# Optimization experiments

Hardware: AMD Instinct MI355X
Metric: run time of the kernel (lower is better)

## Reference

```python
import jax, jax.numpy as jnp
import numpy as np

WINDOW = 20  # window_size from init

def setup_inputs() -> dict:
    key = jax.random.key(0)
    ks = jax.random.split(key, 8)
    B, K, L, H = 8, 64, 1024, 256
    FFN = 3 * H * 4  # input_dim*ffn_ratio
    cand_span_reps = jax.random.normal(ks[0], (B, K, H), dtype=jnp.float32)
    token_reps = jax.random.normal(ks[1], (B, L, H), dtype=jnp.float32)
    W1 = jax.random.normal(ks[2], (3 * H, FFN), dtype=jnp.float32) * (1.0 / np.sqrt(3 * H))
    b1 = jnp.zeros((FFN,), dtype=jnp.float32)
    W2 = jax.random.normal(ks[3], (FFN, H), dtype=jnp.float32) * (1.0 / np.sqrt(FFN))
    b2 = jnp.zeros((H,), dtype=jnp.float32)
    cand_span_ids = jnp.sort(jax.random.randint(ks[4], (B, K, 2), 0, L), axis=-1)
    token_masks = jnp.ones((B, L), dtype=bool)
    return {"cand_span_reps": cand_span_reps, "token_reps": token_reps,
            "W1": W1, "b1": b1, "W2": W2, "b2": b2,
            "cand_span_ids": cand_span_ids, "token_masks": token_masks}

def _span_window_max(token_reps, span_ids, token_masks, window):
    # token_reps: [B,L,H]; span_ids: [B,K,2]; token_masks: [B,L]
    L = token_reps.shape[1]
    seq = jnp.arange(L)[None, None, :]                      # [1,1,L]
    start = span_ids[:, :, 0][:, :, None]                   # [B,K,1]
    end = span_ids[:, :, 1][:, :, None]                     # [B,K,1]
    mask = (((seq >= start - window) & (seq < start)) |
            ((seq > end) & (seq <= end + window)))
    mask = mask & token_masks[:, None, :]                   # [B,K,L]
    # masked max over L -> [B,K,H]
    filled = jnp.where(mask[..., None], token_reps[:, None, :, :], -jnp.inf)
    return jnp.max(filled, axis=2)

def reference(cand_span_reps, token_reps, W1, b1, W2, b2, cand_span_ids, token_masks):
    B, K, H = cand_span_reps.shape
    # Per-span pooled window context [B,K,H]. The pairwise context over the
    # UNION of head & tail windows equals the elementwise max of the two
    # per-span window maxes (max over A|B == max(max A, max B)).
    ctx = _span_window_max(token_reps, cand_span_ids, token_masks, WINDOW)
    context_reps = jnp.maximum(ctx[:, :, None, :], ctx[:, None, :, :])   # [B,K,K,H]
    head_reps = jnp.broadcast_to(cand_span_reps[:, :, None, :], (B, K, K, H))
    tail_reps = jnp.broadcast_to(cand_span_reps[:, None, :, :], (B, K, K, H))
    rel = jnp.concatenate([head_reps, tail_reps, context_reps], axis=-1)  # [B,K,K,3H]
    h = jax.nn.relu(jnp.einsum('bijd,df->bijf', rel, W1) + b1)
    out = jnp.einsum('bijf,fh->bijh', h, W2) + b2
    return out.reshape(B, K * K, H)
```

## Files before the change

kernel.cpp:

```cpp
#include <hip/hip_runtime.h>
#include <hip/hip_bf16.h>
#include <cstdint>
#include <cstddef>


typedef __attribute__((ext_vector_type(8))) short short8;
typedef __attribute__((ext_vector_type(4))) float f32x4;
typedef __attribute__((ext_vector_type(2))) unsigned int u32x2;

#define B_DIM 8
#define K_DIM 64
#define H_DIM 256
#define L_DIM 1024
#define FFN_DIM 3072
#define WINDOW 20

__device__ __forceinline__ unsigned short f2b(float f) {
  unsigned int u = __float_as_uint(f);
  unsigned int r = (u + 0x7FFFu + ((u >> 16) & 1u)) >> 16;
  return (unsigned short)r;
}
__device__ __forceinline__ float b2f(unsigned short h) {
  return __uint_as_float(((unsigned int)h) << 16);
}
__device__ __forceinline__ f32x4 zero4() {
  f32x4 z = {0.f, 0.f, 0.f, 0.f};
  return z;
}
__device__ __forceinline__ void gload_lds16(const void* g, void* l) {
  __builtin_amdgcn_global_load_lds(
      (const __attribute__((address_space(1))) void*)g,
      (__attribute__((address_space(3))) void*)l, 16, 0, 0);
}
__device__ __forceinline__ unsigned int cvt_pk_bf16(float lo, float hi) {
  unsigned int r;
  asm("v_cvt_pk_bf16_f32 %0, %1, %2" : "=v"(r) : "v"(lo), "v"(hi));
  return r;
}


__global__ void cvt_bf16_kernel(const float* __restrict__ in,
                                unsigned short* __restrict__ out, int n) {
  int i = blockIdx.x * blockDim.x + threadIdx.x;
  if (i < n) out[i] = f2b(in[i]);
}

__global__ void transpose_cvt_kernel(const float* __restrict__ in,
                                     unsigned short* __restrict__ out,
                                     int R, int C) {
  __shared__ float t[64][65];
  int c0 = blockIdx.x * 64, r0 = blockIdx.y * 64;
  int tr = threadIdx.x >> 6, tc = threadIdx.x & 63;
  for (int rr = tr; rr < 64; rr += 4)
    t[rr][tc] = in[(size_t)(r0 + rr) * C + (c0 + tc)];
  __syncthreads();
  for (int cc = tr; cc < 64; cc += 4)
    out[(size_t)(c0 + cc) * R + (r0 + tc)] = f2b(t[tc][cc]);
}

__global__ void ctx_kernel(const float* __restrict__ token,
                           const int* __restrict__ ids,
                           unsigned short* __restrict__ ctx) {
  int bk = blockIdx.x;
  int b = bk >> 6;
  int h = threadIdx.x;
  int s = ids[bk * 2 + 0];
  int e = ids[bk * 2 + 1];
  const float* tb = token + ((size_t)b * L_DIM) * H_DIM + h;
  float m = -INFINITY;
  int lo = s - WINDOW; if (lo < 0) lo = 0;
  for (int l2 = lo; l2 < s; ++l2) m = fmaxf(m, tb[(size_t)l2 * H_DIM]);
  int hi = e + WINDOW; if (hi > L_DIM - 1) hi = L_DIM - 1;
  for (int l2 = e + 1; l2 <= hi; ++l2) m = fmaxf(m, tb[(size_t)l2 * H_DIM]);
  ctx[(size_t)bk * H_DIM + h] = f2b(m);
}

__global__ __launch_bounds__(256) void at_gemm_kernel(
    const unsigned short* __restrict__ candb,
    const unsigned short* __restrict__ w1abt,
    const float* __restrict__ b1, float* __restrict__ AT) {
  int n0 = blockIdx.x * 64;
  int r0 = blockIdx.y * 64;
  __shared__ __align__(16) unsigned short A[64 * 256];
  int w = threadIdx.x >> 6, l = threadIdx.x & 63;
  int l15 = l & 15, l4 = l >> 4;
  {
    int row = w * 16 + l15;
    const short8* src = (const short8*)(candb + (size_t)(r0 + row) * H_DIM);
    #pragma unroll
    for (int t = 0; t < 8; ++t) {
      int u = l4 + 4 * t;
      short8 v = src[u];
      *(short8*)(A + row * 256 + ((u ^ (row & 7)) * 8)) = v;
    }
  }
  __syncthreads();
  f32x4 acc[4] = {zero4(), zero4(), zero4(), zero4()};
  int n = n0 + 16 * w + l15;
  const unsigned short* bp = w1abt + (size_t)n * H_DIM + l4 * 8;
  #pragma unroll
  for (int kk = 0; kk < 8; ++kk) {
    short8 bfrag = *(const short8*)(bp + kk * 32);
    #pragma unroll
    for (int rf = 0; rf < 4; ++rf) {
      int row = rf * 16 + l15;
      int u = kk * 4 + l4;
      short8 afrag = *(const short8*)(A + row * 256 + ((u ^ (row & 7)) * 8));
      acc[rf] = __builtin_amdgcn_mfma_f32_16x16x32_bf16(afrag, bfrag, acc[rf], 0, 0, 0);
    }
  }
  float bias = (n < FFN_DIM) ? b1[n] : 0.0f;
  #pragma unroll
  for (int rf = 0; rf < 4; ++rf) {
    #pragma unroll
    for (int qq = 0; qq < 4; ++qq) {
      int row = r0 + rf * 16 + l4 * 4 + qq;
      AT[(size_t)row * (2 * FFN_DIM) + n] = acc[rf][qq] + bias;
    }
  }
}

__global__ __launch_bounds__(1024, 4) void fused_kernel(
    const unsigned short* __restrict__ ctx,
    const unsigned short* __restrict__ w1ct,
    const unsigned short* __restrict__ w2t,
    const float* __restrict__ AT,
    const float* __restrict__ b2,
    float* __restrict__ out) {
  int blk = blockIdx.x;
  blk = (blk & 7) * 32 + (blk >> 3);
  int b = blk >> 5, qp = blk & 31;

  __shared__ __align__(16) char W1s[3 * 16384];
  __shared__ __align__(16) char W2s4[4 * 16384];
  __shared__ __align__(16) char HcS[2 * 8192];

  int tid = threadIdx.x;
  int w = tid >> 6, l = tid & 63;
  int l15 = l & 15, l4 = l >> 4;
  int wl = l15 & 7;
  int s3 = (l15 >> 1) & 3;

  if (w < 8) {
    int wf = w & 1, wj2 = w >> 1;
    int i_w = 2 * qp + (wj2 >> 1);
    int jloc = 32 * (wj2 & 1) + l15;

    short8 bfr[8][2];
    {
      const unsigned short* cb = ctx + ((size_t)b * K_DIM) * H_DIM;
      const unsigned short* ci = cb + (size_t)i_w * H_DIM;
      #pragma unroll
      for (int kk = 0; kk < 8; ++kk) {
        int hoff = kk * 32 + l4 * 8;
        short8 vi = *(const short8*)(ci + hoff);
        #pragma unroll
        for (int jb = 0; jb < 2; ++jb) {
          short8 vj = *(const short8*)(cb + (size_t)(jloc + jb * 16) * H_DIM + hoff);
          short8 vm;
          #pragma unroll
          for (int e = 0; e < 8; ++e) {
            float fa = b2f((unsigned short)vi[e]);
            float fb = b2f((unsigned short)vj[e]);
            vm[e] = (fa >= fb) ? vi[e] : vj[e];
          }
          bfr[kk][jb] = vm;
        }
      }
    }

    int tid_p = (w << 6) | l;
    int fr = tid_p >> 5, u32i = tid_p & 31;
    int offW1 = fr * 512 + (((u32i & 24) | ((u32i & 7) ^ (fr & 7))) << 4);

    int baseA = (16 * wf + l15) * 512;
    int offAe = ((l4 ^ wl) << 4);
    int offAo = (((4 + l4) ^ wl) << 4);
    int colw = 32 * wj2 + l15;
    int uW = 2 * wf + (l4 >> 1);
    int offHw = colw * 64 + ((uW ^ s3) << 4) + ((l4 & 1) << 3);

    const float* avp = AT + (size_t)(b * K_DIM + i_w) * (2 * FFN_DIM) + 16 * wf + 4 * l4;
    const float* tvp = AT + (size_t)(b * K_DIM + jloc) * (2 * FFN_DIM) + FFN_DIM + 16 * wf + 4 * l4;

    auto stageW1 = [&](int c, int buf) {
      const char* g = (const char*)w1ct + (size_t)c * 16384 + offW1;
      char* d = &W1s[buf * 16384 + tid_p * 16];
      gload_lds16(g, d);
      gload_lds16(g + 8192, d + 8192);
    };

    stageW1(0, 0);
    stageW1(1, 1);
    __builtin_amdgcn_sched_barrier(0);
    asm volatile("s_waitcnt vmcnt(2)" ::: "memory");
    __builtin_amdgcn_sched_barrier(0);
    __builtin_amdgcn_s_barrier();
    __builtin_amdgcn_sched_barrier(0);

    int rb = 0, sb = 2;
    for (int c = 0; c <= 96; ++c) {
      f32x4 av = zero4(), tv0 = zero4(), tv1 = zero4();
      if (c < 96) {
        av  = *(const f32x4*)(avp + c * 32);
        tv0 = *(const f32x4*)(tvp + c * 32);
        tv1 = *(const f32x4*)(tvp + 98304 + c * 32);
      }
      __builtin_amdgcn_sched_barrier(0);
      stageW1(c + 2 > 95 ? 95 : c + 2, sb);
      __builtin_amdgcn_sched_barrier(0);

      if (c < 96) {
        const char* w1p = &W1s[rb * 16384 + baseA];
        f32x4 acc1[2] = {zero4(), zero4()};
        __builtin_amdgcn_s_setprio(1);
        #pragma unroll
        for (int m = 0; m < 4; ++m) {
          short8 afe = *(const short8*)(w1p + m * 128 + offAe);
          acc1[0] = __builtin_amdgcn_mfma_f32_16x16x32_bf16(afe, bfr[2 * m][0], acc1[0], 0, 0, 0);
          acc1[1] = __builtin_amdgcn_mfma_f32_16x16x32_bf16(afe, bfr[2 * m][1], acc1[1], 0, 0, 0);
          short8 afo = *(const short8*)(w1p + m * 128 + offAo);
          acc1[0] = __builtin_amdgcn_mfma_f32_16x16x32_bf16(afo, bfr[2 * m + 1][0], acc1[0], 0, 0, 0);
          acc1[1] = __builtin_amdgcn_mfma_f32_16x16x32_bf16(afo, bfr[2 * m + 1][1], acc1[1], 0, 0, 0);
        }
        __builtin_amdgcn_s_setprio(0);

        char* hw = &HcS[(c & 1) * 8192];
        {
          float v0 = fmaxf(acc1[0][0] + av[0] + tv0[0], 0.0f);
          float v1 = fmaxf(acc1[0][1] + av[1] + tv0[1], 0.0f);
          float v2 = fmaxf(acc1[0][2] + av[2] + tv0[2], 0.0f);
          float v3 = fmaxf(acc1[0][3] + av[3] + tv0[3], 0.0f);
          u32x2 pk;
          pk.x = cvt_pk_bf16(v0, v1);
          pk.y = cvt_pk_bf16(v2, v3);
          *(u32x2*)(hw + offHw) = pk;
        }
        {
          float v0 = fmaxf(acc1[1][0] + av[0] + tv1[0], 0.0f);
          float v1 = fmaxf(acc1[1][1] + av[1] + tv1[1], 0.0f);
          float v2 = fmaxf(acc1[1][2] + av[2] + tv1[2], 0.0f);
          float v3 = fmaxf(acc1[1][3] + av[3] + tv1[3], 0.0f);
          u32x2 pk;
          pk.x = cvt_pk_bf16(v0, v1);
          pk.y = cvt_pk_bf16(v2, v3);
          *(u32x2*)(hw + offHw + 1024) = pk;
        }
      }

      __builtin_amdgcn_sched_barrier(0);
      asm volatile("s_waitcnt vmcnt(2) lgkmcnt(0)" ::: "memory");
      __builtin_amdgcn_sched_barrier(0);
      __builtin_amdgcn_s_barrier();
      __builtin_amdgcn_sched_barrier(0);
      ++rb; if (rb == 3) rb = 0;
      ++sb; if (sb == 3) sb = 0;
    }
  } else {
    int cw = w - 8;
    int ch = cw & 3, cj = cw >> 2;
    int tid_c = (cw << 6) | l;
    int h2 = tid_c >> 2, u2 = tid_c & 3;
    int offW2 = h2 * 6144 + ((u2 ^ ((h2 >> 1) & 3)) << 4);
    int baseW2 = ch * 4096 + l15 * 64 + ((l4 ^ s3) << 4);
    int baseHr = cj * 4096 + l15 * 64 + ((l4 ^ s3) << 4);

    auto stageW2 = [&](int c, int buf) {
      const char* g = (const char*)w2t + (size_t)c * 64 + offW2;
      char* d = &W2s4[buf * 16384 + tid_c * 16];
      gload_lds16(g, d);
      gload_lds16(g + 786432, d + 8192);
    };

    f32x4 accO[4][4];
    #pragma unroll
    for (int cf = 0; cf < 4; ++cf)
      #pragma unroll
      for (int jt = 0; jt < 4; ++jt) accO[cf][jt] = zero4();

    stageW2(0, 0);
    stageW2(1, 1);
    __builtin_amdgcn_sched_barrier(0);
    asm volatile("s_waitcnt vmcnt(2)" ::: "memory");
    __builtin_amdgcn_sched_barrier(0);
    __builtin_amdgcn_s_barrier();
    __builtin_amdgcn_sched_barrier(0);

    for (int c = 0; c <= 96; ++c) {
      stageW2(c + 2 > 95 ? 95 : c + 2, (c + 2) & 3);
      __builtin_amdgcn_sched_barrier(0);

      if (c > 0) {
        const char* w2p = &W2s4[((c - 1) & 3) * 16384];
        const char* hcp = &HcS[((c - 1) & 1) * 8192];
        short8 wfr[4], hbv[4];
        #pragma unroll
        for (int cf = 0; cf < 4; ++cf)
          wfr[cf] = *(const short8*)(w2p + baseW2 + cf * 1024);
        #pragma unroll
        for (int jt = 0; jt < 4; ++jt)
          hbv[jt] = *(const short8*)(hcp + baseHr + jt * 1024);
        __builtin_amdgcn_s_setprio(1);
        #pragma unroll
        for (int cf = 0; cf < 4; ++cf)
          #pragma unroll
          for (int jt = 0; jt < 4; ++jt)
            accO[cf][jt] = __builtin_amdgcn_mfma_f32_16x16x32_bf16(wfr[cf], hbv[jt], accO[cf][jt], 0, 0, 0);
        __builtin_amdgcn_s_setprio(0);
      }

      __builtin_amdgcn_sched_barrier(0);
      asm volatile("s_waitcnt vmcnt(2) lgkmcnt(0)" ::: "memory");
      __builtin_amdgcn_sched_barrier(0);
      __builtin_amdgcn_s_barrier();
      __builtin_amdgcn_sched_barrier(0);
    }

    int ig = 2 * qp + cj;
    f32x4 bv[4];
    #pragma unroll
    for (int cf = 0; cf < 4; ++cf)
      bv[cf] = *(const f32x4*)(b2 + 64 * ch + cf * 16 + 4 * l4);
    #pragma unroll
    for (int jt = 0; jt < 4; ++jt) {
      int j = jt * 16 + l15;
      float* row = out + ((size_t)b * (K_DIM * K_DIM) + (size_t)ig * K_DIM + j) * H_DIM;
      #pragma unroll
      for (int cf = 0; cf < 4; ++cf) {
        f32x4 v = accO[cf][jt] + bv[cf];
        *(f32x4*)(row + 64 * ch + cf * 16 + 4 * l4) = v;
      }
    }
  }
}


extern "C" void kernel_launch(void* const* d_in, const int* in_sizes, int n_in,
                              void* d_out, int out_size, void* d_ws, size_t ws_size,
                              hipStream_t stream) {
  const float* cand  = (const float*)d_in[0];
  const float* token = (const float*)d_in[1];
  const float* W1    = (const float*)d_in[2];
  const float* b1    = (const float*)d_in[3];
  const float* W2    = (const float*)d_in[4];
  const float* b2    = (const float*)d_in[5];
  const int*   ids   = (const int*)d_in[6];
  float* out = (float*)d_out;

  char* ws = (char*)d_ws;
  unsigned short* ctx   = (unsigned short*)(ws);
  unsigned short* candb = (unsigned short*)(ws + 262144);
  unsigned short* w1abt = (unsigned short*)(ws + 524288);
  unsigned short* w1ct  = (unsigned short*)(ws + 3670016);
  unsigned short* w2t   = (unsigned short*)(ws + 5242880);
  float*          AT    = (float*)(ws + 6815744);

  hipLaunchKernelGGL(cvt_bf16_kernel, dim3(512), dim3(256), 0, stream,
                     cand, candb, B_DIM * K_DIM * H_DIM);
  hipLaunchKernelGGL(transpose_cvt_kernel, dim3(48, 4), dim3(256), 0, stream,
                     W1, w1abt, 256, FFN_DIM);
  hipLaunchKernelGGL(transpose_cvt_kernel, dim3(48, 4), dim3(256), 0, stream,
                     W1 + (size_t)256 * FFN_DIM, w1abt + (size_t)FFN_DIM * 256, 256, FFN_DIM);
  hipLaunchKernelGGL(transpose_cvt_kernel, dim3(48, 4), dim3(256), 0, stream,
                     W1 + (size_t)512 * FFN_DIM, w1ct, 256, FFN_DIM);
  hipLaunchKernelGGL(transpose_cvt_kernel, dim3(4, 48), dim3(256), 0, stream,
                     W2, w2t, FFN_DIM, 256);
  hipLaunchKernelGGL(ctx_kernel, dim3(512), dim3(256), 0, stream, token, ids, ctx);
  hipLaunchKernelGGL(at_gemm_kernel, dim3(96, 8), dim3(256), 0, stream,
                     candb, w1abt, b1, AT);
  hipLaunchKernelGGL(fused_kernel, dim3(256), dim3(1024), 0, stream,
                     ctx, w1ct, w2t, AT, b2, out);
}
```

Measured before the change: 198.4 us.

## Split fused FFN kernel into one-row-per-block 512-thread blocks with double buffering

The fused two-layer FFN kernel now assigns one head span i per block with 512 threads (4 producer and 4 consumer waves) instead of two i values per 1024-thread block, doubling the grid to 512 blocks. Weight staging drops from triple/quad buffering to double buffering, the hidden tile buffer becomes single, and the producer-consumer pipeline is lockstepped with two barriers per chunk. This aims to raise occupancy and reduce LDS per block, but each block now streams the full W1/W2 chunk for half as much work, doubling weight traffic and adding synchronisation stalls.

New measurement: 189.5 us. 1.05x faster.

```diff
diff --git a/kernel.cpp b/kernel.cpp
--- a/kernel.cpp
+++ b/kernel.cpp
@@ -120,7 +120,7 @@
   }
 }
 
-__global__ __launch_bounds__(1024, 4) void fused_kernel(
+__global__ __launch_bounds__(512, 4) void fused_kernel(
     const unsigned short* __restrict__ ctx,
     const unsigned short* __restrict__ w1ct,
     const unsigned short* __restrict__ w2t,
@@ -128,12 +128,12 @@
     const float* __restrict__ b2,
     float* __restrict__ out) {
   int blk = blockIdx.x;
-  blk = (blk & 7) * 32 + (blk >> 3);
-  int b = blk >> 5, qp = blk & 31;
-
-  __shared__ __align__(16) char W1s[3 * 16384];
-  __shared__ __align__(16) char W2s4[4 * 16384];
-  __shared__ __align__(16) char HcS[2 * 8192];
+  blk = (blk & 7) * 64 + (blk >> 3);
+  int b = blk >> 6, i = blk & 63;
+
+  __shared__ __align__(16) char W1s[2 * 16384];
+  __shared__ __align__(16) char W2s[2 * 16384];
+  __shared__ __align__(16) char HcS[4096];
 
   int tid = threadIdx.x;
   int w = tid >> 6, l = tid & 63;
@@ -141,15 +141,14 @@
   int wl = l15 & 7;
   int s3 = (l15 >> 1) & 3;
 
-  if (w < 8) {
+  if (w < 4) {
     int wf = w & 1, wj2 = w >> 1;
-    int i_w = 2 * qp + (wj2 >> 1);
-    int jloc = 32 * (wj2 & 1) + l15;
+    int jloc = 32 * wj2 + l15;
 
     short8 bfr[8][2];
     {
       const unsigned short* cb = ctx + ((size_t)b * K_DIM) * H_DIM;
-      const unsigned short* ci = cb + (size_t)i_w * H_DIM;
+      const unsigned short* ci = cb + (size_t)i * H_DIM;
       #pragma unroll
       for (int kk = 0; kk < 8; ++kk) {
         int hoff = kk * 32 + l4 * 8;
@@ -172,105 +171,98 @@
     int tid_p = (w << 6) | l;
     int fr = tid_p >> 5, u32i = tid_p & 31;
     int offW1 = fr * 512 + (((u32i & 24) | ((u32i & 7) ^ (fr & 7))) << 4);
-
-    int baseA = (16 * wf + l15) * 512;
-    int offAe = ((l4 ^ wl) << 4);
-    int offAo = (((4 + l4) ^ wl) << 4);
-    int colw = 32 * wj2 + l15;
-    int uW = 2 * wf + (l4 >> 1);
-    int offHw = colw * 64 + ((uW ^ s3) << 4) + ((l4 & 1) << 3);
-
-    const float* avp = AT + (size_t)(b * K_DIM + i_w) * (2 * FFN_DIM) + 16 * wf + 4 * l4;
-    const float* tvp = AT + (size_t)(b * K_DIM + jloc) * (2 * FFN_DIM) + FFN_DIM + 16 * wf + 4 * l4;
-
     auto stageW1 = [&](int c, int buf) {
       const char* g = (const char*)w1ct + (size_t)c * 16384 + offW1;
       char* d = &W1s[buf * 16384 + tid_p * 16];
       gload_lds16(g, d);
+      gload_lds16(g + 4096, d + 4096);
       gload_lds16(g + 8192, d + 8192);
+      gload_lds16(g + 12288, d + 12288);
     };
 
+    int baseA = (16 * wf + l15) * 512;
+    int offAe = (l4 ^ wl) << 4;
+    int offAo = ((4 + l4) ^ wl) << 4;
+    int uW = 2 * wf + (l4 >> 1);
+    int offHw = jloc * 64 + ((uW ^ s3) << 4) + ((l4 & 1) << 3);
+
+    const float* avp = AT + (size_t)(b * K_DIM + i) * (2 * FFN_DIM) + 16 * wf + 4 * l4;
+    const float* tvp = AT + (size_t)(b * K_DIM + jloc) * (2 * FFN_DIM) + FFN_DIM + 16 * wf + 4 * l4;
+
     stageW1(0, 0);
-    stageW1(1, 1);
-    __builtin_amdgcn_sched_barrier(0);
-    asm volatile("s_waitcnt vmcnt(2)" ::: "memory");
+    __builtin_amdgcn_sched_barrier(0);
+    asm volatile("s_waitcnt vmcnt(0)" ::: "memory");
     __builtin_amdgcn_sched_barrier(0);
     __builtin_amdgcn_s_barrier();
     __builtin_amdgcn_sched_barrier(0);
 
-    int rb = 0, sb = 2;
-    for (int c = 0; c <= 96; ++c) {
-      f32x4 av = zero4(), tv0 = zero4(), tv1 = zero4();
-      if (c < 96) {
-        av  = *(const f32x4*)(avp + c * 32);
-        tv0 = *(const f32x4*)(tvp + c * 32);
-        tv1 = *(const f32x4*)(tvp + 98304 + c * 32);
-      }
-      __builtin_amdgcn_sched_barrier(0);
-      stageW1(c + 2 > 95 ? 95 : c + 2, sb);
-      __builtin_amdgcn_sched_barrier(0);
-
-      if (c < 96) {
-        const char* w1p = &W1s[rb * 16384 + baseA];
-        f32x4 acc1[2] = {zero4(), zero4()};
-        __builtin_amdgcn_s_setprio(1);
-        #pragma unroll
-        for (int m = 0; m < 4; ++m) {
-          short8 afe = *(const short8*)(w1p + m * 128 + offAe);
-          acc1[0] = __builtin_amdgcn_mfma_f32_16x16x32_bf16(afe, bfr[2 * m][0], acc1[0], 0, 0, 0);
-          acc1[1] = __builtin_amdgcn_mfma_f32_16x16x32_bf16(afe, bfr[2 * m][1], acc1[1], 0, 0, 0);
-          short8 afo = *(const short8*)(w1p + m * 128 + offAo);
-          acc1[0] = __builtin_amdgcn_mfma_f32_16x16x32_bf16(afo, bfr[2 * m + 1][0], acc1[0], 0, 0, 0);
-          acc1[1] = __builtin_amdgcn_mfma_f32_16x16x32_bf16(afo, bfr[2 * m + 1][1], acc1[1], 0, 0, 0);
-        }
-        __builtin_amdgcn_s_setprio(0);
-
-        char* hw = &HcS[(c & 1) * 8192];
-        {
-          float v0 = fmaxf(acc1[0][0] + av[0] + tv0[0], 0.0f);
-          float v1 = fmaxf(acc1[0][1] + av[1] + tv0[1], 0.0f);
-          float v2 = fmaxf(acc1[0][2] + av[2] + tv0[2], 0.0f);
-          float v3 = fmaxf(acc1[0][3] + av[3] + tv0[3], 0.0f);
-          u32x2 pk;
-          pk.x = cvt_pk_bf16(v0, v1);
-          pk.y = cvt_pk_bf16(v2, v3);
-          *(u32x2*)(hw + offHw) = pk;
-        }
-        {
-          float v0 = fmaxf(acc1[1][0] + av[0] + tv1[0], 0.0f);
-          float v1 = fmaxf(acc1[1][1] + av[1] + tv1[1], 0.0f);
-          float v2 = fmaxf(acc1[1][2] + av[2] + tv1[2], 0.0f);
-          float v3 = fmaxf(acc1[1][3] + av[3] + tv1[3], 0.0f);
-          u32x2 pk;
-          pk.x = cvt_pk_bf16(v0, v1);
-          pk.y = cvt_pk_bf16(v2, v3);
-          *(u32x2*)(hw + offHw + 1024) = pk;
-        }
-      }
-
-      __builtin_amdgcn_sched_barrier(0);
-      asm volatile("s_waitcnt vmcnt(2) lgkmcnt(0)" ::: "memory");
+    for (int c = 0; c < 96; ++c) {
+      f32x4 av  = *(const f32x4*)(avp + c * 32);
+      f32x4 tv0 = *(const f32x4*)(tvp + c * 32);
+      f32x4 tv1 = *(const f32x4*)(tvp + 16 * (2 * FFN_DIM) + c * 32);
+      __builtin_amdgcn_sched_barrier(0);
+      stageW1(c < 95 ? c + 1 : 95, (c + 1) & 1);
+      __builtin_amdgcn_sched_barrier(0);
+
+      const char* w1p = &W1s[(c & 1) * 16384 + baseA];
+      f32x4 acc1[2] = {zero4(), zero4()};
+      __builtin_amdgcn_s_setprio(1);
+      #pragma unroll
+      for (int m = 0; m < 4; ++m) {
+        short8 afe = *(const short8*)(w1p + m * 128 + offAe);
+        acc1[0] = __builtin_amdgcn_mfma_f32_16x16x32_bf16(afe, bfr[2 * m][0], acc1[0], 0, 0, 0);
+        acc1[1] = __builtin_amdgcn_mfma_f32_16x16x32_bf16(afe, bfr[2 * m][1], acc1[1], 0, 0, 0);
+        short8 afo = *(const short8*)(w1p + m * 128 + offAo);
+        acc1[0] = __builtin_amdgcn_mfma_f32_16x16x32_bf16(afo, bfr[2 * m + 1][0], acc1[0], 0, 0, 0);
+        acc1[1] = __builtin_amdgcn_mfma_f32_16x16x32_bf16(afo, bfr[2 * m + 1][1], acc1[1], 0, 0, 0);
+      }
+      __builtin_amdgcn_s_setprio(0);
+
+      {
+        float v0 = fmaxf(acc1[0][0] + av[0] + tv0[0], 0.0f);
+        float v1 = fmaxf(acc1[0][1] + av[1] + tv0[1], 0.0f);
+        float v2 = fmaxf(acc1[0][2] + av[2] + tv0[2], 0.0f);
+        float v3 = fmaxf(acc1[0][3] + av[3] + tv0[3], 0.0f);
+        u32x2 pk;
+        pk.x = cvt_pk_bf16(v0, v1);
+        pk.y = cvt_pk_bf16(v2, v3);
+        *(u32x2*)(HcS + offHw) = pk;
+      }
+      {
+        float v0 = fmaxf(acc1[1][0] + av[0] + tv1[0], 0.0f);
+        float v1 = fmaxf(acc1[1][1] + av[1] + tv1[1], 0.0f);
+        float v2 = fmaxf(acc1[1][2] + av[2] + tv1[2], 0.0f);
+        float v3 = fmaxf(acc1[1][3] + av[3] + tv1[3], 0.0f);
+        u32x2 pk;
+        pk.x = cvt_pk_bf16(v0, v1);
+        pk.y = cvt_pk_bf16(v2, v3);
+        *(u32x2*)(HcS + offHw + 1024) = pk;
+      }
+      __builtin_amdgcn_sched_barrier(0);
+      asm volatile("s_waitcnt lgkmcnt(0)" ::: "memory");
       __builtin_amdgcn_sched_barrier(0);
       __builtin_amdgcn_s_barrier();
       __builtin_amdgcn_sched_barrier(0);
-      ++rb; if (rb == 3) rb = 0;
-      ++sb; if (sb == 3) sb = 0;
+      asm volatile("s_waitcnt vmcnt(0)" ::: "memory");
+      __builtin_amdgcn_sched_barrier(0);
+      __builtin_amdgcn_s_barrier();
+      __builtin_amdgcn_sched_barrier(0);
     }
   } else {
-    int cw = w - 8;
-    int ch = cw & 3, cj = cw >> 2;
-    int tid_c = (cw << 6) | l;
+    int ch = w - 4;
+    int tid_c = (ch << 6) | l;
     int h2 = tid_c >> 2, u2 = tid_c & 3;
     int offW2 = h2 * 6144 + ((u2 ^ ((h2 >> 1) & 3)) << 4);
-    int baseW2 = ch * 4096 + l15 * 64 + ((l4 ^ s3) << 4);
-    int baseHr = cj * 4096 + l15 * 64 + ((l4 ^ s3) << 4);
-
     auto stageW2 = [&](int c, int buf) {
       const char* g = (const char*)w2t + (size_t)c * 64 + offW2;
-      char* d = &W2s4[buf * 16384 + tid_c * 16];
+      char* d = &W2s[buf * 16384 + tid_c * 16];
       gload_lds16(g, d);
-      gload_lds16(g + 786432, d + 8192);
+      gload_lds16(g + 1 * 393216, d + 4096);
+      gload_lds16(g + 2 * 393216, d + 8192);
+      gload_lds16(g + 3 * 393216, d + 12288);
     };
+    int baseW2 = ch * 4096 + l15 * 64 + ((l4 ^ s3) << 4);
+    int baseHr = l15 * 64 + ((l4 ^ s3) << 4);
 
     f32x4 accO[4][4];
     #pragma unroll
@@ -279,44 +271,43 @@
       for (int jt = 0; jt < 4; ++jt) accO[cf][jt] = zero4();
 
     stageW2(0, 0);
-    stageW2(1, 1);
-    __builtin_amdgcn_sched_barrier(0);
-    asm volatile("s_waitcnt vmcnt(2)" ::: "memory");
+    __builtin_amdgcn_sched_barrier(0);
+    asm volatile("s_waitcnt vmcnt(0)" ::: "memory");
     __builtin_amdgcn_sched_barrier(0);
     __builtin_amdgcn_s_barrier();
     __builtin_amdgcn_sched_barrier(0);
 
-    for (int c = 0; c <= 96; ++c) {
-      stageW2(c + 2 > 95 ? 95 : c + 2, (c + 2) & 3);
-      __builtin_amdgcn_sched_barrier(0);
-
-      if (c > 0) {
-        const char* w2p = &W2s4[((c - 1) & 3) * 16384];
-        const char* hcp = &HcS[((c - 1) & 1) * 8192];
-        short8 wfr[4], hbv[4];
-        #pragma unroll
-        for (int cf = 0; cf < 4; ++cf)
-          wfr[cf] = *(const short8*)(w2p + baseW2 + cf * 1024);
+    for (int c = 0; c < 96; ++c) {
+      stageW2(c < 95 ? c + 1 : 95, (c + 1) & 1);
+      __builtin_amdgcn_sched_barrier(0);
+      asm volatile("s_waitcnt vmcnt(4)" ::: "memory");
+      __builtin_amdgcn_sched_barrier(0);
+      __builtin_amdgcn_s_barrier();
+      __builtin_amdgcn_sched_barrier(0);
+
+      const char* w2p = &W2s[(c & 1) * 16384];
+      short8 wfr[4], hbv[4];
+      #pragma unroll
+      for (int cf = 0; cf < 4; ++cf)
+        wfr[cf] = *(const short8*)(w2p + baseW2 + cf * 1024);
+      #pragma unroll
+      for (int jt = 0; jt < 4; ++jt)
+        hbv[jt] = *(const short8*)(HcS + baseHr + jt * 1024);
+      __builtin_amdgcn_s_setprio(1);
+      #pragma unroll
+      for (int cf = 0; cf < 4; ++cf)
         #pragma unroll
         for (int jt = 0; jt < 4; ++jt)
-          hbv[jt] = *(const short8*)(hcp + baseHr + jt * 1024);
-        __builtin_amdgcn_s_setprio(1);
-        #pragma unroll
-        for (int cf = 0; cf < 4; ++cf)
-          #pragma unroll
-          for (int jt = 0; jt < 4; ++jt)
-            accO[cf][jt] = __builtin_amdgcn_mfma_f32_16x16x32_bf16(wfr[cf], hbv[jt], accO[cf][jt], 0, 0, 0);
-        __builtin_amdgcn_s_setprio(0);
-      }
-
-      __builtin_amdgcn_sched_barrier(0);
-      asm volatile("s_waitcnt vmcnt(2) lgkmcnt(0)" ::: "memory");
+          accO[cf][jt] = __builtin_amdgcn_mfma_f32_16x16x32_bf16(wfr[cf], hbv[jt], accO[cf][jt], 0, 0, 0);
+      __builtin_amdgcn_s_setprio(0);
+
+      __builtin_amdgcn_sched_barrier(0);
+      asm volatile("s_waitcnt lgkmcnt(0)" ::: "memory");
       __builtin_amdgcn_sched_barrier(0);
       __builtin_amdgcn_s_barrier();
       __builtin_amdgcn_sched_barrier(0);
     }
 
-    int ig = 2 * qp + cj;
     f32x4 bv[4];
     #pragma unroll
     for (int cf = 0; cf < 4; ++cf)
@@ -324,7 +315,7 @@
     #pragma unroll
     for (int jt = 0; jt < 4; ++jt) {
       int j = jt * 16 + l15;
-      float* row = out + ((size_t)b * (K_DIM * K_DIM) + (size_t)ig * K_DIM + j) * H_DIM;
+      float* row = out + ((size_t)b * (K_DIM * K_DIM) + (size_t)i * K_DIM + j) * H_DIM;
       #pragma unroll
       for (int cf = 0; cf < 4; ++cf) {
         f32x4 v = accO[cf][jt] + bv[cf];
@@ -368,6 +359,6 @@
   hipLaunchKernelGGL(ctx_kernel, dim3(512), dim3(256), 0, stream, token, ids, ctx);
   hipLaunchKernelGGL(at_gemm_kernel, dim3(96, 8), dim3(256), 0, stream,
                      candb, w1abt, b1, AT);
-  hipLaunchKernelGGL(fused_kernel, dim3(256), dim3(1024), 0, stream,
+  hipLaunchKernelGGL(fused_kernel, dim3(512), dim3(512), 0, stream,
                      ctx, w1ct, w2t, AT, b2, out);
 }
```
